# Kernel optimization log

Hardware: AMD Instinct MI355X
Metric: run time of the kernel (lower is better)

The kernel has to match this reference:

```python
import jax, jax.numpy as jnp
import numpy as np

T = 10
EPS = 1e-05

def setup_inputs() -> dict:
    key = jax.random.key(0)
    k1, k2 = jax.random.split(key)
    B, C, H, W = 128, 64, 56, 56
    X = jax.random.normal(k1, (B, C, H, W), dtype=jnp.float32)
    beta = jnp.zeros((C,), dtype=jnp.float32)
    return {"X": X, "beta": beta}


def reference(X, beta):
    # Training-path of BWItnBlock.forward (grad enabled branch of iter_norm_batch)
    B, C, H, W = X.shape
    d = C                      # n_channels, num_groups g = 1
    m = B * H * W
    # x = X.transpose(0,1).view(g, d, -1)  -> [d, m] with g=1
    x = jnp.transpose(X, (1, 0, 2, 3)).reshape(d, m)
    mean = jnp.mean(x, axis=1, keepdims=True)          # [d, 1]
    xc = x - mean                                      # [d, m]
    I = jnp.eye(d, dtype=X.dtype)
    # Sigma = eps*I + xc xc^T / m
    Sigma = EPS * I + (xc @ xc.T) / m                  # [d, d]
    # fix_cov: multiply off-diagonal by 0.9, diagonal by 1.0
    fix = 0.9 + 0.1 * I
    Sigma = Sigma * fix
    rTr = 1.0 / jnp.trace(Sigma)                       # scalar (sum(Sigma * I))
    Sigma_N = Sigma * rTr
    # Newton-Schulz iterations for inverse sqrt: P <- 1.5 P - 0.5 P^3 Sigma_N
    P = I
    for _ in range(T):
        P = 1.5 * P - 0.5 * ((P @ P @ P) @ Sigma_N)
    wm = P * jnp.sqrt(rTr)                             # whitening matrix [d, d]
    xn = wm @ xc                                       # [d, m]
    X_hat = jnp.transpose(xn.reshape(C, B, H, W), (1, 0, 2, 3))
    X_hat = X_hat + beta.reshape(1, C, 1, 1)
    return X_hat
```

## Files before the change

### kernel.cpp

```cpp
#include <hip/hip_runtime.h>

#define CH 64
#define HW 3136
#define MTOT 401408
#define TPX 128
#define NBLK 392
#define TPB 8

typedef __attribute__((ext_vector_type(8))) short short8;
typedef __attribute__((ext_vector_type(4))) float f32x4;
typedef __attribute__((ext_vector_type(4))) unsigned int u32x4;

__device__ __forceinline__ void split8(const float4 a, const float4 b,
                                       short8& hi, short8& lo, float& ssum){
  const float f[8] = {a.x,a.y,a.z,a.w, b.x,b.y,b.z,b.w};
  u32x4 hp, lp;
#pragma unroll
  for (int j=0;j<4;++j){
    const unsigned int b0 = __float_as_uint(f[2*j]);
    const unsigned int b1 = __float_as_uint(f[2*j+1]);
    hp[j] = (b0 >> 16) | (b1 & 0xFFFF0000u);
    const float h0 = __uint_as_float(b0 & 0xFFFF0000u);
    const float h1 = __uint_as_float(b1 & 0xFFFF0000u);
    const unsigned int l0 = __float_as_uint(f[2*j]   - h0);
    const unsigned int l1 = __float_as_uint(f[2*j+1] - h1);
    lp[j] = (l0 >> 16) | (l1 & 0xFFFF0000u);
  }
  hi = __builtin_bit_cast(short8, hp);
  lo = __builtin_bit_cast(short8, lp);
  ssum += ((f[0]+f[1])+(f[2]+f[3])) + ((f[4]+f[5])+(f[6]+f[7]));
}

__global__ __launch_bounds__(256) void k1_cov(const float* __restrict__ X,
                                              float* __restrict__ SR){
  constexpr int RG[10] = {0,1,1,2,2,2,3,3,3,3};
  constexpr int CG[10] = {0,0,1,0,1,2,0,1,2,3};
  __shared__ __align__(16) float buf[2][64*TPX];
  __shared__ float chs[64];

  const int t   = threadIdx.x;
  const int wid = __builtin_amdgcn_readfirstlane(t >> 6);
  const int l   = t & 63;
  const int lr  = l & 15;
  const int q   = l >> 4;

  f32x4 acc[10];
#pragma unroll
  for (int bi=0; bi<10; ++bi) acc[bi] = (f32x4){0.f,0.f,0.f,0.f};
  float sums[4] = {0.f,0.f,0.f,0.f};

  auto stage = [&](int tl, float* dst){
    const unsigned mbase = (unsigned)(blockIdx.x*TPB + tl) * TPX;
#pragma unroll
    for (int j=0;j<8;++j){
      const int r  = 16*wid + 2*j + (l>>5);
      const int cb = (l&31) ^ (r&7);
      const unsigned m  = mbase + 4*cb;
      const unsigned b  = m / HW;
      const unsigned hw = m - b*HW;
      const float* src = X + (size_t)b*(CH*HW) + (size_t)r*HW + hw;
      __builtin_amdgcn_global_load_lds(
        (const __attribute__((address_space(1))) unsigned int*)src,
        (__attribute__((address_space(3))) unsigned int*)(dst + (16*wid + 2*j)*TPX),
        16, 0, 0);
    }
  };

  stage(0, buf[0]);
  asm volatile("s_waitcnt vmcnt(0)" ::: "memory");
  __syncthreads();

  int pb = 0;
  for (int tl=0; tl<TPB; ++tl){
    if (tl+1 < TPB) stage(tl+1, buf[pb^1]);
    const char* bp = (const char*)buf[pb];
    short8 fh[4], fl[4];
#pragma unroll
    for (int g=0; g<4; ++g){
      const int r   = 16*g + lr;
      const int sw  = r & 7;
      const int cb0 = 8*wid + 2*q;
      const float4 v0 = *(const float4*)(bp + r*512 + 16*((cb0+0)^sw));
      const float4 v1 = *(const float4*)(bp + r*512 + 16*((cb0+1)^sw));
      split8(v0, v1, fh[g], fl[g], sums[g]);
    }
#pragma unroll
    for (int bi=0; bi<10; ++bi){
      acc[bi] = __builtin_amdgcn_mfma_f32_16x16x32_bf16(fh[RG[bi]], fh[CG[bi]], acc[bi], 0,0,0);
      acc[bi] = __builtin_amdgcn_mfma_f32_16x16x32_bf16(fh[RG[bi]], fl[CG[bi]], acc[bi], 0,0,0);
      acc[bi] = __builtin_amdgcn_mfma_f32_16x16x32_bf16(fl[RG[bi]], fh[CG[bi]], acc[bi], 0,0,0);
    }
    asm volatile("s_waitcnt vmcnt(0)" ::: "memory");
    __syncthreads();
    pb ^= 1;
  }

#pragma unroll
  for (int g=0; g<4; ++g){
    sums[g] += __shfl_xor(sums[g], 16);
    sums[g] += __shfl_xor(sums[g], 32);
  }

  float* red = &buf[0][0];
  for (int w=0; w<4; ++w){
    if (wid == w){
#pragma unroll
      for (int bi=0; bi<10; ++bi){
        const int row0 = RG[bi]*16 + 4*q;
        const int col  = CG[bi]*16 + lr;
#pragma unroll
        for (int r=0; r<4; ++r){
          float* d = &red[(row0+r)*64 + col];
          if (w==0) *d = acc[bi][r]; else *d += acc[bi][r];
        }
      }
      if (l < 16){
#pragma unroll
        for (int g=0; g<4; ++g){
          if (w==0) chs[g*16+l] = sums[g]; else chs[g*16+l] += sums[g];
        }
      }
    }
    __syncthreads();
  }

#pragma unroll
  for (int bi=0; bi<10; ++bi){
    const int r = RG[bi]*16 + (t>>4);
    const int c = CG[bi]*16 + (t&15);
    unsafeAtomicAdd(&SR[r*64+c], red[r*64+c]);
  }
  if (t < 64) unsafeAtomicAdd(&SR[4096+t], chs[t]);
}

__device__ __forceinline__ void mm_AtB(const float* a, const float* b, float* out,
                                       float alpha, const float* aff, float beta_){
  const int t = threadIdx.x;
  const int c2 = 2*(t & 31);
  const int r0 = 8*(t >> 5);
  float acc[8][2];
#pragma unroll
  for (int i=0;i<8;++i){ acc[i][0]=0.f; acc[i][1]=0.f; }
  for (int k=0;k<64;++k){
    const float2 bv = *(const float2*)&b[k*64 + c2];
    const float4 a0 = *(const float4*)&a[k*64 + r0];
    const float4 a1 = *(const float4*)&a[k*64 + r0 + 4];
    const float av[8] = {a0.x,a0.y,a0.z,a0.w, a1.x,a1.y,a1.z,a1.w};
#pragma unroll
    for (int i=0;i<8;++i){ acc[i][0] += av[i]*bv.x; acc[i][1] += av[i]*bv.y; }
  }
  float res[8][2];
#pragma unroll
  for (int i=0;i<8;++i){
    float f0 = alpha*acc[i][0], f1 = alpha*acc[i][1];
    if (aff){ f0 += beta_*aff[(r0+i)*64 + c2]; f1 += beta_*aff[(r0+i)*64 + c2 + 1]; }
    res[i][0]=f0; res[i][1]=f1;
  }
  __syncthreads();
#pragma unroll
  for (int i=0;i<8;++i){
    float2 o2; o2.x = res[i][0]; o2.y = res[i][1];
    *(float2*)&out[(r0+i)*64 + c2] = o2;
  }
  __syncthreads();
}

__global__ __launch_bounds__(256) void k2_wm(const float* __restrict__ SR,
                                             const float* __restrict__ beta,
                                             float* __restrict__ WMT,
                                             float* __restrict__ OFS){
  __shared__ __align__(16) float bufE[4096];
  __shared__ __align__(16) float bufA[4096];
  __shared__ __align__(16) float bufB[4096];
  __shared__ float meanv[64];
  __shared__ float scal[2];
  const int t = threadIdx.x;
  const float inv_m = 1.f/(float)MTOT;
  if (t < 64) meanv[t] = SR[4096 + t]*inv_m;
  __syncthreads();
  for (int idx=t; idx<4096; idx+=256){
    const int r = idx >> 6, c = idx & 63;
    const int src = ((r >> 4) >= (c >> 4)) ? idx : (c*64 + r);
    const float cov = SR[src]*inv_m - meanv[r]*meanv[c];
    bufE[idx] = (r==c) ? (cov + 1e-5f - 1.f) : 0.9f*cov;
  }
  __syncthreads();
  float n2 = 0.f, tr = 0.f;
  for (int idx=t; idx<4096; idx+=256){
    const float e = bufE[idx];
    n2 += e*e;
    if ((idx >> 6) == (idx & 63)) tr += e;
  }
  bufA[t] = n2; bufB[t] = tr;
  __syncthreads();
  if (t < 64){
    bufA[t] = bufA[t]+bufA[t+64]+bufA[t+128]+bufA[t+192];
    bufB[t] = bufB[t]+bufB[t+64]+bufB[t+128]+bufB[t+192];
  }
  __syncthreads();
  if (t == 0){
    float s1=0.f, s2=0.f;
    for (int i=0;i<64;++i){ s1 += bufA[i]; s2 += bufB[i]; }
    scal[0] = s1; scal[1] = s2;
  }
  __syncthreads();
  const float frob2 = scal[0];
  const float trE   = scal[1];
  float wscale = 1.f;
  const float* wmLds;
  if (frob2 < 0.04f){
    mm_AtB(bufE, bufE, bufA, 1.f, nullptr, 0.f);
    mm_AtB(bufA, bufE, bufB, 1.f, nullptr, 0.f);
    for (int idx=t; idx<4096; idx+=256){
      const int r = idx >> 6, c = idx & 63;
      bufB[idx] = ((r==c)?1.f:0.f) - 0.5f*bufE[idx] + 0.375f*bufA[idx] - 0.3125f*bufB[idx];
    }
    mm_AtB(bufA, bufA, bufE, 1.f, nullptr, 0.f);
    for (int idx=t; idx<4096; idx+=256)
      bufB[idx] += 0.2734375f*bufE[idx];
    wmLds = bufB;
  } else {
    const float rTr = 1.f/(trE + 64.f);
    for (int idx=t; idx<4096; idx+=256){
      const int r = idx >> 6, c = idx & 63;
      bufE[idx] = (bufE[idx] + ((r==c)?1.f:0.f))*rTr;
      bufA[idx] = (r==c)?1.f:0.f;
    }
    __syncthreads();
    for (int it=0; it<10; ++it){
      mm_AtB(bufA, bufE, bufB, 1.f, nullptr, 0.f);
      mm_AtB(bufA, bufB, bufB, 1.f, nullptr, 0.f);
      mm_AtB(bufA, bufB, bufA, -0.5f, bufA, 1.5f);
    }
    wscale = sqrtf(rTr);
    wmLds = bufA;
  }
  __syncthreads();
  for (int idx=t; idx<4096; idx+=256)
    WMT[(idx & 63)*64 + (idx >> 6)] = wmLds[idx]*wscale;
  if (t < 64){
    float d = 0.f;
    for (int j=0;j<64;++j) d += wmLds[t*64 + j]*meanv[j];
    OFS[t] = beta[t] - d*wscale;
  }
}

__global__ __launch_bounds__(256) void k3_apply(const float* __restrict__ X,
                                                const float* __restrict__ WMT,
                                                const float* __restrict__ OFS,
                                                float* __restrict__ out){
  __shared__ __align__(16) float buf[2][64*TPX];
  const int t = threadIdx.x;
  const int w = __builtin_amdgcn_readfirstlane((int)(t >> 6));
  const int l = t & 63;
  const int c0 = 16*w;

  float ofs[16];
#pragma unroll
  for (int i=0;i<16;++i) ofs[i] = OFS[c0+i];

  auto stage = [&](int tl, float* dst){
    const unsigned mbase = (unsigned)(blockIdx.x*TPB + tl) * TPX;
#pragma unroll
    for (int j=0;j<8;++j){
      const int r  = 16*w + 2*j + (l>>5);
      const unsigned m  = mbase + 4*(l&31);
      const unsigned b  = m / HW;
      const unsigned hw = m - b*HW;
      const float* src = X + (size_t)b*(CH*HW) + (size_t)r*HW + hw;
      __builtin_amdgcn_global_load_lds(
        (const __attribute__((address_space(1))) unsigned int*)src,
        (__attribute__((address_space(3))) unsigned int*)(dst + (16*w + 2*j)*TPX),
        16, 0, 0);
    }
  };

  stage(0, buf[0]);
  asm volatile("s_waitcnt vmcnt(0)" ::: "memory");
  __syncthreads();

  int pb = 0;
  for (int tl=0; tl<TPB; ++tl){
    if (tl+1 < TPB) stage(tl+1, buf[pb^1]);
    const float* bp = buf[pb];
    float acc[16][2];
#pragma unroll
    for (int i=0;i<16;++i){ acc[i][0]=0.f; acc[i][1]=0.f; }
    for (int k=0;k<64;++k){
      const float2 xv = *(const float2*)&bp[k*TPX + 2*l];
      const float* wr = &WMT[k*64 + c0];
#pragma unroll
      for (int i=0;i<16;++i){
        acc[i][0] += wr[i]*xv.x;
        acc[i][1] += wr[i]*xv.y;
      }
    }
    {
      const unsigned P2 = (unsigned)(blockIdx.x*TPB + tl)*TPX + 2*l;
      const unsigned b2 = P2 / HW;
      const unsigned hw2 = P2 - b2*HW;
      float* ob = out + (size_t)b2*(CH*HW) + hw2;
#pragma unroll
      for (int i=0;i<16;++i){
        float2 pk; pk.x = acc[i][0]+ofs[i]; pk.y = acc[i][1]+ofs[i];
        *(float2*)(ob + (size_t)(c0+i)*HW) = pk;
      }
    }
    asm volatile("s_waitcnt vmcnt(0)" ::: "memory");
    __syncthreads();
    pb ^= 1;
  }
}

extern "C" void kernel_launch(void* const* d_in, const int* in_sizes, int n_in,
                              void* d_out, int out_size, void* d_ws, size_t ws_size,
                              hipStream_t stream){
  const float* X    = (const float*)d_in[0];
  const float* beta = (const float*)d_in[1];
  float* out = (float*)d_out;
  float* ws  = (float*)d_ws;
  float* SR  = ws;
  float* WMT = ws + 4160;
  float* OFS = WMT + 4096;
  hipMemsetAsync(SR, 0, 4160*sizeof(float), stream);
  hipLaunchKernelGGL(k1_cov,   dim3(NBLK), dim3(256), 0, stream, X, SR);
  hipLaunchKernelGGL(k2_wm,    dim3(1),    dim3(256), 0, stream, SR, beta, WMT, OFS);
  hipLaunchKernelGGL(k3_apply, dim3(NBLK), dim3(256), 0, stream, X, WMT, OFS, out);
}
```

Baseline: 260.1 us.

## Rewrite apply kernel with split-bf16 MFMA and retune covariance grid

The apply kernel's scalar FMA loop over an LDS-staged tile is replaced by MFMA 16x16x32 bf16 instructions. Both the whitening matrix and X are split into high and low bf16 parts so three MFMAs recover near-fp32 accuracy. Each block now handles 128 pixels with direct strided global loads and no LDS staging, launched over 3136 blocks. The covariance kernel grid doubles to 784 blocks with half the tiles each, and k2 now writes the whitening matrix untransposed. The aim is to cut ALU time in the apply pass, at the cost of uncoalesced per-lane column loads and stores.

```diff
diff --git a/kernel.cpp b/kernel.cpp
--- a/kernel.cpp
+++ b/kernel.cpp
@@ -4,8 +4,8 @@
 #define HW 3136
 #define MTOT 401408
 #define TPX 128
-#define NBLK 392
-#define TPB 8
+#define K1_NBLK 784
+#define K1_TPB 4
 
 typedef __attribute__((ext_vector_type(8))) short short8;
 typedef __attribute__((ext_vector_type(4))) float f32x4;
@@ -50,7 +50,7 @@
   float sums[4] = {0.f,0.f,0.f,0.f};
 
   auto stage = [&](int tl, float* dst){
-    const unsigned mbase = (unsigned)(blockIdx.x*TPB + tl) * TPX;
+    const unsigned mbase = (unsigned)(blockIdx.x*K1_TPB + tl) * TPX;
 #pragma unroll
     for (int j=0;j<8;++j){
       const int r  = 16*wid + 2*j + (l>>5);
@@ -71,8 +71,8 @@
   __syncthreads();
 
   int pb = 0;
-  for (int tl=0; tl<TPB; ++tl){
-    if (tl+1 < TPB) stage(tl+1, buf[pb^1]);
+  for (int tl=0; tl<K1_TPB; ++tl){
+    if (tl+1 < K1_TPB) stage(tl+1, buf[pb^1]);
     const char* bp = (const char*)buf[pb];
     short8 fh[4], fl[4];
 #pragma unroll
@@ -167,7 +167,7 @@
 
 __global__ __launch_bounds__(256) void k2_wm(const float* __restrict__ SR,
                                              const float* __restrict__ beta,
-                                             float* __restrict__ WMT,
+                                             float* __restrict__ WM,
                                              float* __restrict__ OFS){
   __shared__ __align__(16) float bufE[4096];
   __shared__ __align__(16) float bufA[4096];
@@ -236,8 +236,7 @@
     wmLds = bufA;
   }
   __syncthreads();
-  for (int idx=t; idx<4096; idx+=256)
-    WMT[(idx & 63)*64 + (idx >> 6)] = wmLds[idx]*wscale;
+  for (int idx=t; idx<4096; idx+=256) WM[idx] = wmLds[idx]*wscale;
   if (t < 64){
     float d = 0.f;
     for (int j=0;j<64;++j) d += wmLds[t*64 + j]*meanv[j];
@@ -246,69 +245,76 @@
 }
 
 __global__ __launch_bounds__(256) void k3_apply(const float* __restrict__ X,
-                                                const float* __restrict__ WMT,
+                                                const float* __restrict__ WM,
                                                 const float* __restrict__ OFS,
                                                 float* __restrict__ out){
-  __shared__ __align__(16) float buf[2][64*TPX];
-  const int t = threadIdx.x;
-  const int w = __builtin_amdgcn_readfirstlane((int)(t >> 6));
-  const int l = t & 63;
-  const int c0 = 16*w;
-
-  float ofs[16];
-#pragma unroll
-  for (int i=0;i<16;++i) ofs[i] = OFS[c0+i];
-
-  auto stage = [&](int tl, float* dst){
-    const unsigned mbase = (unsigned)(blockIdx.x*TPB + tl) * TPX;
-#pragma unroll
-    for (int j=0;j<8;++j){
-      const int r  = 16*w + 2*j + (l>>5);
-      const unsigned m  = mbase + 4*(l&31);
-      const unsigned b  = m / HW;
-      const unsigned hw = m - b*HW;
-      const float* src = X + (size_t)b*(CH*HW) + (size_t)r*HW + hw;
-      __builtin_amdgcn_global_load_lds(
-        (const __attribute__((address_space(1))) unsigned int*)src,
-        (__attribute__((address_space(3))) unsigned int*)(dst + (16*w + 2*j)*TPX),
-        16, 0, 0);
-    }
-  };
-
-  stage(0, buf[0]);
-  asm volatile("s_waitcnt vmcnt(0)" ::: "memory");
-  __syncthreads();
-
-  int pb = 0;
-  for (int tl=0; tl<TPB; ++tl){
-    if (tl+1 < TPB) stage(tl+1, buf[pb^1]);
-    const float* bp = buf[pb];
-    float acc[16][2];
-#pragma unroll
-    for (int i=0;i<16;++i){ acc[i][0]=0.f; acc[i][1]=0.f; }
-    for (int k=0;k<64;++k){
-      const float2 xv = *(const float2*)&bp[k*TPX + 2*l];
-      const float* wr = &WMT[k*64 + c0];
-#pragma unroll
-      for (int i=0;i<16;++i){
-        acc[i][0] += wr[i]*xv.x;
-        acc[i][1] += wr[i]*xv.y;
+  const int t   = threadIdx.x;
+  const int wid = __builtin_amdgcn_readfirstlane(t >> 6);
+  const int l   = t & 63;
+  const int lr  = l & 15;
+  const int q   = l >> 4;
+
+  short8 ah[4][2], al[4][2];
+  float dummy = 0.f;
+#pragma unroll
+  for (int cb=0; cb<4; ++cb)
+#pragma unroll
+    for (int ks=0; ks<2; ++ks){
+      const float* wp = WM + (16*cb + lr)*64 + ks*32 + q*8;
+      const float4 w0 = *(const float4*)wp;
+      const float4 w1 = *(const float4*)(wp + 4);
+      split8(w0, w1, ah[cb][ks], al[cb][ks], dummy);
+    }
+
+  unsigned bb[2], hwp[2];
+#pragma unroll
+  for (int pbk=0; pbk<2; ++pbk){
+    const unsigned px = (unsigned)blockIdx.x*128u + 32u*wid + 16u*pbk + lr;
+    bb[pbk]  = px / HW;
+    hwp[pbk] = px - bb[pbk]*HW;
+  }
+
+  f32x4 acc[4][2];
+#pragma unroll
+  for (int cb=0; cb<4; ++cb)
+#pragma unroll
+    for (int pbk=0; pbk<2; ++pbk) acc[cb][pbk] = (f32x4){0.f,0.f,0.f,0.f};
+
+#pragma unroll
+  for (int ks=0; ks<2; ++ks){
+    short8 bh[2], bl[2];
+#pragma unroll
+    for (int pbk=0; pbk<2; ++pbk){
+      const float* xb = X + (size_t)bb[pbk]*(CH*HW) + hwp[pbk] + (size_t)(ks*32 + q*8)*HW;
+      float f[8];
+#pragma unroll
+      for (int j=0;j<8;++j) f[j] = xb[(size_t)j*HW];
+      const float4 v0 = {f[0],f[1],f[2],f[3]};
+      const float4 v1 = {f[4],f[5],f[6],f[7]};
+      split8(v0, v1, bh[pbk], bl[pbk], dummy);
+    }
+#pragma unroll
+    for (int cb=0; cb<4; ++cb)
+#pragma unroll
+      for (int pbk=0; pbk<2; ++pbk){
+        acc[cb][pbk] = __builtin_amdgcn_mfma_f32_16x16x32_bf16(ah[cb][ks], bh[pbk], acc[cb][pbk], 0,0,0);
+        acc[cb][pbk] = __builtin_amdgcn_mfma_f32_16x16x32_bf16(ah[cb][ks], bl[pbk], acc[cb][pbk], 0,0,0);
+        acc[cb][pbk] = __builtin_amdgcn_mfma_f32_16x16x32_bf16(al[cb][ks], bh[pbk], acc[cb][pbk], 0,0,0);
       }
-    }
-    {
-      const unsigned P2 = (unsigned)(blockIdx.x*TPB + tl)*TPX + 2*l;
-      const unsigned b2 = P2 / HW;
-      const unsigned hw2 = P2 - b2*HW;
-      float* ob = out + (size_t)b2*(CH*HW) + hw2;
-#pragma unroll
-      for (int i=0;i<16;++i){
-        float2 pk; pk.x = acc[i][0]+ofs[i]; pk.y = acc[i][1]+ofs[i];
-        *(float2*)(ob + (size_t)(c0+i)*HW) = pk;
-      }
-    }
-    asm volatile("s_waitcnt vmcnt(0)" ::: "memory");
-    __syncthreads();
-    pb ^= 1;
+  }
+
+#pragma unroll
+  for (int cb=0; cb<4; ++cb){
+    float ofs[4];
+#pragma unroll
+    for (int r=0;r<4;++r) ofs[r] = OFS[16*cb + 4*q + r];
+#pragma unroll
+    for (int pbk=0; pbk<2; ++pbk){
+      float* ob = out + (size_t)bb[pbk]*(CH*HW) + hwp[pbk] + (size_t)(16*cb + 4*q)*HW;
+#pragma unroll
+      for (int r=0;r<4;++r)
+        ob[(size_t)r*HW] = acc[cb][pbk][r] + ofs[r];
+    }
   }
 }
 
@@ -320,10 +326,10 @@
   float* out = (float*)d_out;
   float* ws  = (float*)d_ws;
   float* SR  = ws;
-  float* WMT = ws + 4160;
-  float* OFS = WMT + 4096;
+  float* WM  = ws + 4160;
+  float* OFS = WM + 4096;
   hipMemsetAsync(SR, 0, 4160*sizeof(float), stream);
-  hipLaunchKernelGGL(k1_cov,   dim3(NBLK), dim3(256), 0, stream, X, SR);
-  hipLaunchKernelGGL(k2_wm,    dim3(1),    dim3(256), 0, stream, SR, beta, WMT, OFS);
-  hipLaunchKernelGGL(k3_apply, dim3(NBLK), dim3(256), 0, stream, X, WMT, OFS, out);
-}
+  hipLaunchKernelGGL(k1_cov,   dim3(K1_NBLK), dim3(256), 0, stream, X, SR);
+  hipLaunchKernelGGL(k2_wm,    dim3(1),       dim3(256), 0, stream, SR, beta, WM, OFS);
+  hipLaunchKernelGGL(k3_apply, dim3(3136),    dim3(256), 0, stream, X, WM, OFS, out);
+}
```

Result: faster. 230.4 us (-11.4%).
